# Performance work log

Hardware: AMD Instinct MI355X
Metric: run time of the kernel (lower is better)

## Reference

```python
import jax, jax.numpy as jnp
import numpy as np

NEG = -10000.0

def setup_inputs() -> dict:
    key = jax.random.key(0)
    ks = jax.random.split(key, 8)
    B, S, D = 16, 1024, 768
    scale = 1.0 / np.sqrt(D)
    return {
        "q": jax.random.normal(ks[0], (B, S, D), jnp.float32),
        "k": jax.random.normal(ks[1], (B, S, D), jnp.float32),
        "v": jax.random.normal(ks[2], (B, S, D), jnp.float32),
        "Wq": jax.random.normal(ks[3], (D, D), jnp.float32) * scale,
        "bq": jnp.zeros((D,), jnp.float32),
        "Wk": jax.random.normal(ks[4], (D, D), jnp.float32) * scale,
        "bk": jnp.zeros((D,), jnp.float32),
        "Wv": jax.random.normal(ks[5], (D, D), jnp.float32) * scale,
        "bv": jnp.zeros((D,), jnp.float32),
        "temperature": jnp.float32(1.0),
    }

def reference(q, k, v, Wq, bq, Wk, bk, Wv, bv, temperature):
    # Linear projections (torch Linear: x @ W.T + b; here W stored as [out,in])
    Q = jnp.einsum("bsd,ed->bse", q, Wq) + bq  # [B,S,Dq]
    K = jnp.einsum("bsd,ed->bse", k, Wk) + bk  # [B,S,Dk]
    V = jnp.einsum("bsd,ed->bse", v, Wv) + bv  # [B,S,Dv]
    scores = jnp.einsum("bqe,bke->bqk", Q, K) / temperature  # [B,S,S]
    S = scores.shape[-1]
    diag = jnp.eye(S, dtype=bool)  # diagonal self-exclusion mask
    scores = jnp.where(diag[None, :, :], NEG, scores)
    attn = jax.nn.softmax(scores, axis=-1)
    return jnp.einsum("bqk,bke->bqe", attn, V)
```

## Files before the change

### kernel.cpp

```cpp
#include <hip/hip_runtime.h>
#include <hip/hip_bf16.h>
#include <math.h>


typedef _Float16 f16x8 __attribute__((ext_vector_type(8)));
typedef _Float16 f16x4 __attribute__((ext_vector_type(4)));
typedef __attribute__((ext_vector_type(4))) float f32x4;

template<typename T>
__device__ __forceinline__ void async_copy16(T* lds, const T* g) {
    __builtin_amdgcn_global_load_lds(
        (const __attribute__((address_space(1))) unsigned int*)g,
        (__attribute__((address_space(3))) unsigned int*)lds, 16, 0, 0);
}

#define BM 128
#define BN 128
#define BK 32

template<int EPI, int BIAS>
__global__ __launch_bounds__(256, 2)
void mfma_gemm(const _Float16* __restrict__ A, const _Float16* __restrict__ B,
               const float* __restrict__ bias,
               void* __restrict__ C0,
               int K, int lda, int ldb, int ldc,
               long long sA, long long sB, long long sC)
{
    __shared__ _Float16 sAh[BM * BK];
    __shared__ _Float16 sBh[BN * BK];

    const int tid = threadIdx.x;

    const int gx = gridDim.x, gy = gridDim.y;
    const int nwg = gx * gy * gridDim.z;
    const int p = blockIdx.x + gx * (blockIdx.y + gy * blockIdx.z);
    const int cpx = nwg >> 3;
    const int l = (nwg & 7) ? p : (p & 7) * cpx + (p >> 3);
    const int bx = l % gx;
    const int by = (l / gx) % gy;
    const long long bz = l / (gx * gy);

    const int m0 = by * BM;
    const int n0 = bx * BN;

    const _Float16* A0 = A + bz * sA;
    const _Float16* B0 = B + bz * sB;

    const int lrow  = tid >> 2;
    const int lslot = tid & 3;

    const int lane = tid & 63;
    const int wv   = tid >> 6;
    const int wm   = wv >> 1, wn = wv & 1;
    const int fr   = lane & 15;
    const int fs   = lane >> 4;
    const int sw   = fs ^ (fr & 3);
    const int abase = (wm * 64 + fr) * BK + sw * 8;
    const int bbase = (wn * 64 + fr) * BK + sw * 8;

    f32x4 acc[4][4] = {};

    for (int kt = 0; kt < K; kt += BK) {
        #pragma unroll
        for (int it = 0; it < 2; ++it) {
            const int row = lrow + it * 64;
            const int gsl = (lslot ^ (row & 3)) << 3;
            const size_t loff = (size_t)tid * 8 + (size_t)it * 2048;
            async_copy16(&sAh[loff], A0 + (size_t)(m0 + row) * lda + kt + gsl);
            async_copy16(&sBh[loff], B0 + (size_t)(n0 + row) * ldb + kt + gsl);
        }
        __syncthreads();

        f16x8 ah[4], bh[4];
        #pragma unroll
        for (int i = 0; i < 4; ++i) {
            ah[i] = *(const f16x8*)&sAh[abase + i * 512];
            bh[i] = *(const f16x8*)&sBh[bbase + i * 512];
        }
        #pragma unroll
        for (int mi = 0; mi < 4; ++mi)
            #pragma unroll
            for (int ni = 0; ni < 4; ++ni)
                acc[mi][ni] = __builtin_amdgcn_mfma_f32_16x16x32_f16(
                    ah[mi], bh[ni], acc[mi][ni], 0, 0, 0);
        __syncthreads();
    }

    const int er = fs * 4;
    #pragma unroll
    for (int mi = 0; mi < 4; ++mi) {
        #pragma unroll
        for (int ni = 0; ni < 4; ++ni) {
            const int col = n0 + wn * 64 + ni * 16 + fr;
            #pragma unroll
            for (int r = 0; r < 4; ++r) {
                const int row = m0 + wm * 64 + mi * 16 + er + r;
                float vv = acc[mi][ni][r];
                if (BIAS == 1) vv += bias[col];
                if (BIAS == 2) vv += bias[row];
                const size_t idx = (size_t)bz * sC + (size_t)row * ldc + col;
                if (EPI == 0) ((float*)C0)[idx] = vv;
                else          ((_Float16*)C0)[idx] = (_Float16)vv;
            }
        }
    }
}

__global__ __launch_bounds__(256)
void tof16_kernel(const float* __restrict__ src, _Float16* __restrict__ dst,
                  long long n)
{
    long long i = ((long long)blockIdx.x * 256 + threadIdx.x) * 8;
    const long long stride = (long long)gridDim.x * 2048;
    for (; i < n; i += stride) {
        const float4 a = *(const float4*)&src[i];
        const float4 b = *(const float4*)&src[i + 4];
        f16x8 o;
        o[0] = (_Float16)a.x; o[1] = (_Float16)a.y;
        o[2] = (_Float16)a.z; o[3] = (_Float16)a.w;
        o[4] = (_Float16)b.x; o[5] = (_Float16)b.y;
        o[6] = (_Float16)b.z; o[7] = (_Float16)b.w;
        *(f16x8*)&dst[i] = o;
    }
}

__global__ __launch_bounds__(256)
void transpose_f16(const float* __restrict__ src, _Float16* __restrict__ dst, int n)
{
    __shared__ float t[64][65];
    const int tx = threadIdx.x & 63, ty = threadIdx.x >> 6;
    const int r0 = blockIdx.y * 64, c0 = blockIdx.x * 64;
    #pragma unroll
    for (int r = 0; r < 16; ++r) {
        const int row = ty * 16 + r;
        t[row][tx] = src[(size_t)(r0 + row) * n + c0 + tx];
    }
    __syncthreads();
    #pragma unroll
    for (int r = 0; r < 16; ++r) {
        const int orow = ty * 16 + r;
        dst[(size_t)(c0 + orow) * n + r0 + tx] = (_Float16)t[tx][orow];
    }
}

__global__ __launch_bounds__(256)
void colvec_kernel(const _Float16* __restrict__ WkT, const float* __restrict__ bq,
                   float* __restrict__ colvec, int n)
{
    const int wv = threadIdx.x >> 6, lane = threadIdx.x & 63;
    const int d = blockIdx.x * 4 + wv;
    float s = 0.f;
    for (int e = lane; e < n; e += 64)
        s += (float)WkT[(size_t)d * n + e] * bq[e];
    #pragma unroll
    for (int off = 32; off; off >>= 1) s += __shfl_down(s, off, 64);
    if (lane == 0) colvec[d] = s;
}

__global__ __launch_bounds__(256)
void cterm_kernel(const float* __restrict__ k, const float* __restrict__ colvec,
                  float* __restrict__ cterm)
{
    const int wv = threadIdx.x >> 6, lane = threadIdx.x & 63;
    const long long row = (long long)blockIdx.x * 4 + wv;
    const float* kp = k + row * 768;
    float s = 0.f;
    #pragma unroll
    for (int i = 0; i < 3; ++i) {
        const float4 a = *(const float4*)&kp[lane * 4 + i * 256];
        const float4 c = *(const float4*)&colvec[lane * 4 + i * 256];
        s += a.x * c.x + a.y * c.y + a.z * c.z + a.w * c.w;
    }
    #pragma unroll
    for (int off = 32; off; off >>= 1) s += __shfl_down(s, off, 64);
    if (lane == 0) cterm[row] = s;
}

__global__ __launch_bounds__(256)
void softmax_diag(float* __restrict__ P, const float* __restrict__ tptr,
                  const float* __restrict__ cterm, int S)
{
    const int row = blockIdx.x;
    const int i   = row % S;
    float* rp = P + (long long)row * S;
    const int tid = threadIdx.x;
    const float invt = 1.0f / tptr[0];

    const float4 v  = *(const float4*)&rp[tid * 4];
    const float4 ct = *(const float4*)&cterm[(long long)(row / S) * S + tid * 4];
    float vals[4] = {v.x + ct.x, v.y + ct.y, v.z + ct.z, v.w + ct.w};
    #pragma unroll
    for (int j = 0; j < 4; ++j) {
        vals[j] *= invt;
        if (tid * 4 + j == i) vals[j] = -INFINITY;
    }

    float mx = fmaxf(fmaxf(vals[0], vals[1]), fmaxf(vals[2], vals[3]));
    #pragma unroll
    for (int off = 32; off > 0; off >>= 1)
        mx = fmaxf(mx, __shfl_down(mx, off, 64));

    __shared__ float smax[4], ssum[4];
    const int wv = tid >> 6, ln = tid & 63;
    if (ln == 0) smax[wv] = mx;
    __syncthreads();
    mx = fmaxf(fmaxf(smax[0], smax[1]), fmaxf(smax[2], smax[3]));

    float e[4];
    float s = 0.f;
    #pragma unroll
    for (int j = 0; j < 4; ++j) { e[j] = expf(vals[j] - mx); s += e[j]; }
    #pragma unroll
    for (int off = 32; off > 0; off >>= 1)
        s += __shfl_down(s, off, 64);
    if (ln == 0) ssum[wv] = s;
    __syncthreads();
    s = ssum[0] + ssum[1] + ssum[2] + ssum[3];

    const float inv = 1.0f / s;
    f16x4 o;
    o[0] = (_Float16)(e[0] * inv);
    o[1] = (_Float16)(e[1] * inv);
    o[2] = (_Float16)(e[2] * inv);
    o[3] = (_Float16)(e[3] * inv);
    *(f16x4*)&((_Float16*)rp)[tid * 4] = o;
}

extern "C" void kernel_launch(void* const* d_in, const int* in_sizes, int n_in,
                              void* d_out, int out_size, void* d_ws, size_t ws_size,
                              hipStream_t stream)
{
    const float* q    = (const float*)d_in[0];
    const float* k    = (const float*)d_in[1];
    const float* v    = (const float*)d_in[2];
    const float* Wq   = (const float*)d_in[3];
    const float* bq   = (const float*)d_in[4];
    const float* Wk   = (const float*)d_in[5];
    const float* bk   = (const float*)d_in[6];
    const float* Wv   = (const float*)d_in[7];
    const float* bv   = (const float*)d_in[8];
    const float* temp = (const float*)d_in[9];
    (void)bk;

    const int S = 1024, D = 768;
    const long long nE = 16LL * S * D;
    const long long nW = (long long)D * D;

    char* ws = (char*)d_ws;
    _Float16* qh  = (_Float16*)(ws + 0);
    _Float16* kh  = (_Float16*)(ws + 25165824);
    _Float16* vh  = (_Float16*)(ws + 50331648);
    _Float16* VT  = (_Float16*)(ws + 75497472);
    _Float16* KG  = (_Float16*)(ws + 100663296);
    float*  scores = (float*)(ws + 125829120);
    _Float16* wvh = (_Float16*)(ws + 192937984);
    _Float16* WqT = (_Float16*)(ws + 194117632);
    _Float16* WkT = (_Float16*)(ws + 195297280);
    _Float16* G   = (_Float16*)(ws + 196476928);
    float* colvec = (float*)(ws + 197656576);
    float* cterm  = (float*)(ws + 197659648);

    dim3 blk(256);

    tof16_kernel<<<1024, blk, 0, stream>>>(q, qh, nE);
    tof16_kernel<<<1024, blk, 0, stream>>>(k, kh, nE);
    tof16_kernel<<<1024, blk, 0, stream>>>(v, vh, nE);
    tof16_kernel<<<288,  blk, 0, stream>>>(Wv, wvh, nW);
    transpose_f16<<<dim3(12, 12), blk, 0, stream>>>(Wq, WqT, D);
    transpose_f16<<<dim3(12, 12), blk, 0, stream>>>(Wk, WkT, D);

    colvec_kernel<<<192,  blk, 0, stream>>>(WkT, bq, colvec, D);
    cterm_kernel <<<4096, blk, 0, stream>>>(k, colvec, cterm);

    mfma_gemm<1, 2><<<dim3(8, 6, 16), blk, 0, stream>>>(
        wvh, vh, bv, VT,
        768, 768, 768, 1024, 0, (long long)S * D, (long long)D * S);

    mfma_gemm<1, 0><<<dim3(6, 6, 1), blk, 0, stream>>>(
        WqT, WkT, nullptr, G,
        768, 768, 768, 768, 0, 0, 0);

    mfma_gemm<1, 0><<<dim3(6, 128, 1), blk, 0, stream>>>(
        kh, G, nullptr, KG,
        768, 768, 768, 768, 0, 0, 0);

    mfma_gemm<0, 0><<<dim3(8, 8, 16), blk, 0, stream>>>(
        qh, KG, nullptr, scores,
        768, 768, 768, 1024,
        (long long)S * D, (long long)S * D, (long long)S * S);

    softmax_diag<<<16 * S, blk, 0, stream>>>(scores, temp, cterm, S);

    mfma_gemm<0, 0><<<dim3(6, 8, 16), blk, 0, stream>>>(
        (const _Float16*)scores, VT, nullptr, d_out,
        1024, 2048, 1024, 768,
        2LL * S * S, (long long)D * S, (long long)S * D);
}
```

Measured before the change: 246.2 us.

## Triple-buffer GEMM LDS loads and merge q/k/v fp16 conversions into one launch

The MFMA GEMM moves from a single LDS buffer to three rotating buffers. Async global-to-LDS copies for tile t+2 are issued while tile t is computed, with explicit vmcnt/lgkmcnt waits and raw barriers replacing __syncthreads. The three separate fp32-to-fp16 conversion launches for q, k and v are merged into one launch that uses blockIdx.z to pick the tensor. The extra buffers triple LDS use (48KB per block), which may hurt the 2-blocks-per-CU occupancy, and the hand-set vmcnt(4) must match the number of loads in flight.

```diff
diff --git a/kernel.cpp b/kernel.cpp
--- a/kernel.cpp
+++ b/kernel.cpp
@@ -1,5 +1,4 @@
 #include <hip/hip_runtime.h>
-#include <hip/hip_bf16.h>
 #include <math.h>
 
 
@@ -26,8 +25,8 @@
                int K, int lda, int ldb, int ldc,
                long long sA, long long sB, long long sC)
 {
-    __shared__ _Float16 sAh[BM * BK];
-    __shared__ _Float16 sBh[BN * BK];
+    __shared__ _Float16 sA3[3][BM * BK];
+    __shared__ _Float16 sB3[3][BN * BK];
 
     const int tid = threadIdx.x;
 
@@ -58,24 +57,37 @@
     const int abase = (wm * 64 + fr) * BK + sw * 8;
     const int bbase = (wn * 64 + fr) * BK + sw * 8;
 
-    f32x4 acc[4][4] = {};
-
-    for (int kt = 0; kt < K; kt += BK) {
+    const int nt = K / BK;
+
+    auto stage = [&](int buf, int t) {
+        const int kt = t * BK;
         #pragma unroll
         for (int it = 0; it < 2; ++it) {
             const int row = lrow + it * 64;
             const int gsl = (lslot ^ (row & 3)) << 3;
             const size_t loff = (size_t)tid * 8 + (size_t)it * 2048;
-            async_copy16(&sAh[loff], A0 + (size_t)(m0 + row) * lda + kt + gsl);
-            async_copy16(&sBh[loff], B0 + (size_t)(n0 + row) * ldb + kt + gsl);
+            async_copy16(&sA3[buf][loff], A0 + (size_t)(m0 + row) * lda + kt + gsl);
+            async_copy16(&sB3[buf][loff], B0 + (size_t)(n0 + row) * ldb + kt + gsl);
         }
-        __syncthreads();
-
+    };
+
+    f32x4 acc[4][4] = {};
+
+    stage(0, 0);
+    if (nt > 1) stage(1, 1);
+
+    int cb = 0;
+    for (int t = 0; t < nt; ++t) {
+        asm volatile("s_waitcnt vmcnt(4)" ::: "memory");
+        __builtin_amdgcn_s_barrier();
+
+        const _Float16* sa = sA3[cb];
+        const _Float16* sb = sB3[cb];
         f16x8 ah[4], bh[4];
         #pragma unroll
         for (int i = 0; i < 4; ++i) {
-            ah[i] = *(const f16x8*)&sAh[abase + i * 512];
-            bh[i] = *(const f16x8*)&sBh[bbase + i * 512];
+            ah[i] = *(const f16x8*)&sa[abase + i * 512];
+            bh[i] = *(const f16x8*)&sb[bbase + i * 512];
         }
         #pragma unroll
         for (int mi = 0; mi < 4; ++mi)
@@ -83,7 +95,15 @@
             for (int ni = 0; ni < 4; ++ni)
                 acc[mi][ni] = __builtin_amdgcn_mfma_f32_16x16x32_f16(
                     ah[mi], bh[ni], acc[mi][ni], 0, 0, 0);
-        __syncthreads();
+
+        asm volatile("s_waitcnt lgkmcnt(0)" ::: "memory");
+        __builtin_amdgcn_s_barrier();
+
+        if (t + 2 < nt) {
+            const int nb = cb + 2 >= 3 ? cb - 1 : cb + 2;
+            stage(nb, t + 2);
+        }
+        cb = cb + 1 == 3 ? 0 : cb + 1;
     }
 
     const int er = fs * 4;
@@ -107,6 +127,28 @@
 }
 
 __global__ __launch_bounds__(256)
+void tof16_3(const float* __restrict__ q, const float* __restrict__ k,
+             const float* __restrict__ v,
+             _Float16* __restrict__ qh, _Float16* __restrict__ kh,
+             _Float16* __restrict__ vh, long long n)
+{
+    const float* src = blockIdx.z == 0 ? q : blockIdx.z == 1 ? k : v;
+    _Float16* dst    = blockIdx.z == 0 ? qh : blockIdx.z == 1 ? kh : vh;
+    long long i = ((long long)blockIdx.x * 256 + threadIdx.x) * 8;
+    const long long stride = (long long)gridDim.x * 2048;
+    for (; i < n; i += stride) {
+        const float4 a = *(const float4*)&src[i];
+        const float4 b = *(const float4*)&src[i + 4];
+        f16x8 o;
+        o[0] = (_Float16)a.x; o[1] = (_Float16)a.y;
+        o[2] = (_Float16)a.z; o[3] = (_Float16)a.w;
+        o[4] = (_Float16)b.x; o[5] = (_Float16)b.y;
+        o[6] = (_Float16)b.z; o[7] = (_Float16)b.w;
+        *(f16x8*)&dst[i] = o;
+    }
+}
+
+__global__ __launch_bounds__(256)
 void tof16_kernel(const float* __restrict__ src, _Float16* __restrict__ dst,
                   long long n)
 {
@@ -262,10 +304,8 @@
 
     dim3 blk(256);
 
-    tof16_kernel<<<1024, blk, 0, stream>>>(q, qh, nE);
-    tof16_kernel<<<1024, blk, 0, stream>>>(k, kh, nE);
-    tof16_kernel<<<1024, blk, 0, stream>>>(v, vh, nE);
-    tof16_kernel<<<288,  blk, 0, stream>>>(Wv, wvh, nW);
+    tof16_3<<<dim3(2048, 1, 3), blk, 0, stream>>>(q, k, v, qh, kh, vh, nE);
+    tof16_kernel<<<288, blk, 0, stream>>>(Wv, wvh, nW);
     transpose_f16<<<dim3(12, 12), blk, 0, stream>>>(Wq, WqT, D);
     transpose_f16<<<dim3(12, 12), blk, 0, stream>>>(Wk, WkT, D);
 
```

Measured after the change: 246.3 us. No clear change (+0.0%).

## Fuse fp32-to-fp16 input conversion into GEMM loads and double-buffer LDS

Applied to the files above, without the earlier changes.

Removes the three standalone conversion kernels for q, k and v. The GEMMs now read fp32 activations straight from global memory through registers, convert them to fp16 and store them to LDS. The GEMM main loop also moves to a two-stage LDS double buffer, so the next tile is fetched while MFMAs run on the current one. This saves roughly 150MB of extra global traffic and three launches. In exchange, LDS use doubles, register pressure rises, and A/B tiles for the k-projection and scores GEMMs are reloaded as fp32 (twice the bytes per load).

```diff
diff --git a/kernel.cpp b/kernel.cpp
--- a/kernel.cpp
+++ b/kernel.cpp
@@ -1,5 +1,4 @@
 #include <hip/hip_runtime.h>
-#include <hip/hip_bf16.h>
 #include <math.h>
 
 
@@ -18,16 +17,15 @@
 #define BN 128
 #define BK 32
 
-template<int EPI, int BIAS>
+template<int EPI, int BIAS, int CVTA, int CVTB>
 __global__ __launch_bounds__(256, 2)
-void mfma_gemm(const _Float16* __restrict__ A, const _Float16* __restrict__ B,
-               const float* __restrict__ bias,
-               void* __restrict__ C0,
+void mfma_gemm(const void* __restrict__ Ap, const void* __restrict__ Bp,
+               const float* __restrict__ bias, void* __restrict__ C0,
                int K, int lda, int ldb, int ldc,
                long long sA, long long sB, long long sC)
 {
-    __shared__ _Float16 sAh[BM * BK];
-    __shared__ _Float16 sBh[BN * BK];
+    __shared__ _Float16 sA2[2][BM * BK];
+    __shared__ _Float16 sB2[2][BN * BK];
 
     const int tid = threadIdx.x;
 
@@ -43,8 +41,10 @@
     const int m0 = by * BM;
     const int n0 = bx * BN;
 
-    const _Float16* A0 = A + bz * sA;
-    const _Float16* B0 = B + bz * sB;
+    const _Float16* A0h = (const _Float16*)Ap + (CVTA ? 0 : bz * sA);
+    const float*    A0f = (const float*)Ap    + (CVTA ? bz * sA : 0);
+    const _Float16* B0h = (const _Float16*)Bp + (CVTB ? 0 : bz * sB);
+    const float*    B0f = (const float*)Bp    + (CVTB ? bz * sB : 0);
 
     const int lrow  = tid >> 2;
     const int lslot = tid & 3;
@@ -58,24 +58,74 @@
     const int abase = (wm * 64 + fr) * BK + sw * 8;
     const int bbase = (wn * 64 + fr) * BK + sw * 8;
 
-    f32x4 acc[4][4] = {};
-
-    for (int kt = 0; kt < K; kt += BK) {
+    float4 ra[2][2];
+    float4 rb[2][2];
+
+    auto issue = [&](int nb, int t) {
+        const int kt = t * BK;
         #pragma unroll
         for (int it = 0; it < 2; ++it) {
             const int row = lrow + it * 64;
             const int gsl = (lslot ^ (row & 3)) << 3;
             const size_t loff = (size_t)tid * 8 + (size_t)it * 2048;
-            async_copy16(&sAh[loff], A0 + (size_t)(m0 + row) * lda + kt + gsl);
-            async_copy16(&sBh[loff], B0 + (size_t)(n0 + row) * ldb + kt + gsl);
+            if (CVTA) {
+                const float* src = A0f + (size_t)(m0 + row) * lda + kt + gsl;
+                ra[it][0] = *(const float4*)src;
+                ra[it][1] = *(const float4*)(src + 4);
+            } else {
+                async_copy16(&sA2[nb][loff], A0h + (size_t)(m0 + row) * lda + kt + gsl);
+            }
+            if (CVTB) {
+                const float* src = B0f + (size_t)(n0 + row) * ldb + kt + gsl;
+                rb[it][0] = *(const float4*)src;
+                rb[it][1] = *(const float4*)(src + 4);
+            } else {
+                async_copy16(&sB2[nb][loff], B0h + (size_t)(n0 + row) * ldb + kt + gsl);
+            }
         }
-        __syncthreads();
-
+    };
+    auto commit = [&](int nb) {
+        if (!(CVTA || CVTB)) return;
+        #pragma unroll
+        for (int it = 0; it < 2; ++it) {
+            const size_t loff = (size_t)tid * 8 + (size_t)it * 2048;
+            if (CVTA) {
+                f16x8 o;
+                o[0] = (_Float16)ra[it][0].x; o[1] = (_Float16)ra[it][0].y;
+                o[2] = (_Float16)ra[it][0].z; o[3] = (_Float16)ra[it][0].w;
+                o[4] = (_Float16)ra[it][1].x; o[5] = (_Float16)ra[it][1].y;
+                o[6] = (_Float16)ra[it][1].z; o[7] = (_Float16)ra[it][1].w;
+                *(f16x8*)&sA2[nb][loff] = o;
+            }
+            if (CVTB) {
+                f16x8 o;
+                o[0] = (_Float16)rb[it][0].x; o[1] = (_Float16)rb[it][0].y;
+                o[2] = (_Float16)rb[it][0].z; o[3] = (_Float16)rb[it][0].w;
+                o[4] = (_Float16)rb[it][1].x; o[5] = (_Float16)rb[it][1].y;
+                o[6] = (_Float16)rb[it][1].z; o[7] = (_Float16)rb[it][1].w;
+                *(f16x8*)&sB2[nb][loff] = o;
+            }
+        }
+    };
+
+    f32x4 acc[4][4] = {};
+    const int nt = K / BK;
+
+    issue(0, 0);
+    commit(0);
+    __syncthreads();
+
+    int cur = 0;
+    for (int t = 0; t < nt; ++t) {
+        if (t + 1 < nt) issue(cur ^ 1, t + 1);
+
+        const _Float16* sa = sA2[cur];
+        const _Float16* sb = sB2[cur];
         f16x8 ah[4], bh[4];
         #pragma unroll
         for (int i = 0; i < 4; ++i) {
-            ah[i] = *(const f16x8*)&sAh[abase + i * 512];
-            bh[i] = *(const f16x8*)&sBh[bbase + i * 512];
+            ah[i] = *(const f16x8*)&sa[abase + i * 512];
+            bh[i] = *(const f16x8*)&sb[bbase + i * 512];
         }
         #pragma unroll
         for (int mi = 0; mi < 4; ++mi)
@@ -83,7 +133,10 @@
             for (int ni = 0; ni < 4; ++ni)
                 acc[mi][ni] = __builtin_amdgcn_mfma_f32_16x16x32_f16(
                     ah[mi], bh[ni], acc[mi][ni], 0, 0, 0);
+
+        if (t + 1 < nt) commit(cur ^ 1);
         __syncthreads();
+        cur ^= 1;
     }
 
     const int er = fs * 4;
@@ -243,56 +296,49 @@
     (void)bk;
 
     const int S = 1024, D = 768;
-    const long long nE = 16LL * S * D;
     const long long nW = (long long)D * D;
 
     char* ws = (char*)d_ws;
-    _Float16* qh  = (_Float16*)(ws + 0);
-    _Float16* kh  = (_Float16*)(ws + 25165824);
-    _Float16* vh  = (_Float16*)(ws + 50331648);
-    _Float16* VT  = (_Float16*)(ws + 75497472);
-    _Float16* KG  = (_Float16*)(ws + 100663296);
-    float*  scores = (float*)(ws + 125829120);
-    _Float16* wvh = (_Float16*)(ws + 192937984);
-    _Float16* WqT = (_Float16*)(ws + 194117632);
-    _Float16* WkT = (_Float16*)(ws + 195297280);
-    _Float16* G   = (_Float16*)(ws + 196476928);
-    float* colvec = (float*)(ws + 197656576);
-    float* cterm  = (float*)(ws + 197659648);
+    _Float16* VT  = (_Float16*)(ws + 0);
+    _Float16* KG  = (_Float16*)(ws + 25165824);
+    float*  scores = (float*)(ws + 50331648);
+    _Float16* wvh = (_Float16*)(ws + 117440512);
+    _Float16* WqT = (_Float16*)(ws + 118620160);
+    _Float16* WkT = (_Float16*)(ws + 119799808);
+    _Float16* G   = (_Float16*)(ws + 120979456);
+    float* colvec = (float*)(ws + 122159104);
+    float* cterm  = (float*)(ws + 122162176);
 
     dim3 blk(256);
 
-    tof16_kernel<<<1024, blk, 0, stream>>>(q, qh, nE);
-    tof16_kernel<<<1024, blk, 0, stream>>>(k, kh, nE);
-    tof16_kernel<<<1024, blk, 0, stream>>>(v, vh, nE);
-    tof16_kernel<<<288,  blk, 0, stream>>>(Wv, wvh, nW);
+    tof16_kernel<<<288, blk, 0, stream>>>(Wv, wvh, nW);
     transpose_f16<<<dim3(12, 12), blk, 0, stream>>>(Wq, WqT, D);
     transpose_f16<<<dim3(12, 12), blk, 0, stream>>>(Wk, WkT, D);
 
     colvec_kernel<<<192,  blk, 0, stream>>>(WkT, bq, colvec, D);
     cterm_kernel <<<4096, blk, 0, stream>>>(k, colvec, cterm);
 
-    mfma_gemm<1, 2><<<dim3(8, 6, 16), blk, 0, stream>>>(
-        wvh, vh, bv, VT,
+    mfma_gemm<1, 2, 0, 1><<<dim3(8, 6, 16), blk, 0, stream>>>(
+        wvh, v, bv, VT,
         768, 768, 768, 1024, 0, (long long)S * D, (long long)D * S);
 
-    mfma_gemm<1, 0><<<dim3(6, 6, 1), blk, 0, stream>>>(
+    mfma_gemm<1, 0, 0, 0><<<dim3(6, 6, 1), blk, 0, stream>>>(
         WqT, WkT, nullptr, G,
         768, 768, 768, 768, 0, 0, 0);
 
-    mfma_gemm<1, 0><<<dim3(6, 128, 1), blk, 0, stream>>>(
-        kh, G, nullptr, KG,
+    mfma_gemm<1, 0, 1, 0><<<dim3(6, 128, 1), blk, 0, stream>>>(
+        k, G, nullptr, KG,
         768, 768, 768, 768, 0, 0, 0);
 
-    mfma_gemm<0, 0><<<dim3(8, 8, 16), blk, 0, stream>>>(
-        qh, KG, nullptr, scores,
+    mfma_gemm<0, 0, 1, 0><<<dim3(8, 8, 16), blk, 0, stream>>>(
+        q, KG, nullptr, scores,
         768, 768, 768, 1024,
         (long long)S * D, (long long)S * D, (long long)S * S);
 
     softmax_diag<<<16 * S, blk, 0, stream>>>(scores, temp, cterm, S);
 
-    mfma_gemm<0, 0><<<dim3(6, 8, 16), blk, 0, stream>>>(
-        (const _Float16*)scores, VT, nullptr, d_out,
+    mfma_gemm<0, 0, 0, 0><<<dim3(6, 8, 16), blk, 0, stream>>>(
+        scores, VT, nullptr, d_out,
         1024, 2048, 1024, 768,
         2LL * S * S, (long long)D * S, (long long)S * D);
 }
```

Result: no change. 246.3 us (+0.0%).
